# Kernel tuning notes

Measured on AMD Instinct MI355X. Metric: run time of the kernel, lower is better.

## Reference

```python
import jax, jax.numpy as jnp
import numpy as np

N = 384        # number of sentences (paramemory rows)
D = 768        # d_mlp (BERT hidden size)
C = 2          # num_classes


def setup_inputs() -> dict:
    key = jax.random.key(0)
    k1, k2, k3 = jax.random.split(key, 3)
    paramemory = jax.random.normal(k1, (N, D), dtype=jnp.float32)
    # Classifier params (eval mode: dropout p=0.0 -> identity)
    W1 = jax.random.normal(k2, (D, 2 * D), dtype=jnp.float32) * (1.0 / np.sqrt(2 * D))
    b1 = jnp.zeros((D,), dtype=jnp.float32)
    W2 = jax.random.normal(k3, (C, D), dtype=jnp.float32) * (1.0 / np.sqrt(D))
    b2 = jnp.zeros((C,), dtype=jnp.float32)
    return {"paramemory": paramemory, "W1": W1, "b1": b1, "W2": W2, "b2": b2}


def reference(paramemory, W1, b1, W2, b2):
    # Original: cp_mem[i, j] = concat(p[i], p[j]); lin = tanh(cp_mem @ W1.T + b1)
    # Equivalent fused form: split W1 columns into the halves that multiply p[i]
    # and p[j]; the concat+matmul becomes a broadcast-add of two small GEMMs.
    d = paramemory.shape[1]
    A = paramemory @ W1[:, :d].T          # [N, D] contribution of p[i]
    B = paramemory @ W1[:, d:].T          # [N, D] contribution of p[j]
    lin_out = jnp.tanh(A[:, None, :] + B[None, :, :] + b1)  # [N, N, D]
    logits = lin_out @ W2.T + b2          # [N, N, C]
    return logits
```

## Files before the change

kernel.cpp:

```cpp
#include <hip/hip_runtime.h>
#include <stdint.h>

#define NROWS 384
#define DDIM  768
#define NCOL  1536
#define L2E2  2.885390081777927f

#define WS_BT  294912
#define WS_PBF 589824
#define WS_WBF 737280

typedef short bf16x8 __attribute__((ext_vector_type(8)));
typedef float f32x4  __attribute__((ext_vector_type(4)));

__device__ __forceinline__ uint16_t f2bf(float x) {
  const uint32_t u = __float_as_uint(x);
  return (uint16_t)((u + 0x7FFFu + ((u >> 16) & 1u)) >> 16);
}
__device__ __forceinline__ bf16x8 pack8(const float* f) {
  bf16x8 r;
  #pragma unroll
  for (int j = 0; j < 8; ++j) r[j] = (short)f2bf(f[j]);
  return r;
}

__global__ __launch_bounds__(256) void k0_cvt(
    const float* __restrict__ p, const float* __restrict__ W1,
    float* __restrict__ ws) {
  const int t = blockIdx.x * 256 + threadIdx.x;
  const int NP = NROWS * DDIM / 8;
  float f[8];
  if (t < NP) {
    *(float4*)&f[0] = *(const float4*)&p[t * 8];
    *(float4*)&f[4] = *(const float4*)&p[t * 8 + 4];
    *(bf16x8*)((uint16_t*)(ws + WS_PBF) + (size_t)t * 8) = pack8(f);
  } else {
    const int u = t - NP;
    *(float4*)&f[0] = *(const float4*)&W1[(size_t)u * 8];
    *(float4*)&f[4] = *(const float4*)&W1[(size_t)u * 8 + 4];
    *(bf16x8*)((uint16_t*)(ws + WS_WBF) + (size_t)u * 8) = pack8(f);
  }
}

__global__ __launch_bounds__(256) void k1_mfma(
    const float* __restrict__ b1, float* __restrict__ ws) {
  __shared__ float cmb[2][64][4];

  const int lane = threadIdx.x & 63;
  const int w    = threadIdx.x >> 6;
  const int nsub = w & 1;
  const int ksub = w >> 1;
  const int nn   = lane & 15;
  const int quad = lane >> 4;

  const int mbase = blockIdx.y * 16;
  const int nbase = blockIdx.x * 32 + nsub * 16;
  const int g     = nbase >= DDIM;
  const int obase = nbase - g * DDIM;

  const uint16_t* __restrict__ pbf = (const uint16_t*)(ws + WS_PBF);
  const uint16_t* __restrict__ wbf = (const uint16_t*)(ws + WS_WBF);

  const uint16_t* __restrict__ pa =
      pbf + (size_t)(mbase + nn) * DDIM + ksub * 384 + quad * 8;
  const uint16_t* __restrict__ pb =
      wbf + (size_t)(obase + nn) * NCOL + g * DDIM + ksub * 384 + quad * 8;

  f32x4 acc = {0.f, 0.f, 0.f, 0.f};

  #pragma unroll 4
  for (int kk = 0; kk < 384; kk += 32) {
    const bf16x8 a = *(const bf16x8*)&pa[kk];
    const bf16x8 b = *(const bf16x8*)&pb[kk];
    acc = __builtin_amdgcn_mfma_f32_16x16x32_bf16(a, b, acc, 0, 0, 0);
  }

  if (ksub == 1)
    *(float4*)&cmb[nsub][lane][0] = make_float4(acc[0], acc[1], acc[2], acc[3]);
  __syncthreads();
  if (ksub == 0) {
    const float4 o4 = *(const float4*)&cmb[nsub][lane][0];
    float v[4] = {acc[0] + o4.x, acc[1] + o4.y, acc[2] + o4.z, acc[3] + o4.w};
    const int od = obase + nn;
    if (!g) {
      const float bias = b1[od];
      float* __restrict__ A2 = ws;
      #pragma unroll
      for (int r = 0; r < 4; ++r)
        A2[(size_t)(mbase + quad * 4 + r) * DDIM + od] = (v[r] + bias) * L2E2;
    } else {
      float* __restrict__ Bt = ws + WS_BT;
      const int hi = (od >> 2) * NROWS;
      const int lo = od & 3;
      #pragma unroll
      for (int r = 0; r < 4; ++r)
        Bt[(size_t)(hi + mbase + quad * 4 + r) * 4 + lo] = v[r] * L2E2;
    }
  }
}

__global__ __launch_bounds__(256) void k2_fused(
    const float* __restrict__ ws, const float* __restrict__ W2,
    const float* __restrict__ b2, float* __restrict__ out) {
  __shared__ float As[192][16];
  __shared__ float Wsh[192][8];
  __shared__ float part[3][4][64][2];

  const int lane = threadIdx.x & 63;
  const int h    = threadIdx.x >> 6;
  const int i0   = blockIdx.x * 4;
  const int j    = blockIdx.y * 64 + lane;

  for (int u = threadIdx.x; u < 768 + 384; u += 256) {
    if (u < 768) {
      const int row = u / 192, dg = u % 192;
      *(float4*)&As[dg][row * 4] =
          *(const float4*)&ws[(size_t)(i0 + row) * DDIM + dg * 4];
    } else {
      const int v = u - 768, c = v / 192, dg = v % 192;
      *(float4*)&Wsh[dg][c * 4] =
          *(const float4*)&W2[(size_t)c * DDIM + dg * 4];
    }
  }

  const float* __restrict__ w0g = W2 + h * 192;
  const float* __restrict__ w1g = W2 + DDIM + h * 192;
  float sw0 = w0g[lane] + w0g[lane + 64] + w0g[lane + 128];
  float sw1 = w1g[lane] + w1g[lane + 64] + w1g[lane + 128];
  #pragma unroll
  for (int off = 32; off; off >>= 1) {
    sw0 += __shfl_xor(sw0, off);
    sw1 += __shfl_xor(sw1, off);
  }
  __syncthreads();

  const float4* __restrict__ B4 =
      (const float4*)(ws + WS_BT) + (size_t)(h * 48) * NROWS + j;

  f32x4 s0[4] = {{0,0,0,0},{0,0,0,0},{0,0,0,0},{0,0,0,0}};
  f32x4 s1[4] = {{0,0,0,0},{0,0,0,0},{0,0,0,0},{0,0,0,0}};

  #pragma unroll 2
  for (int dg = 0; dg < 48; ++dg) {
    const int dgg = h * 48 + dg;
    const float4 b4  = B4[(size_t)dg * NROWS];
    const float4 w04 = *(const float4*)&Wsh[dgg][0];
    const float4 w14 = *(const float4*)&Wsh[dgg][4];

    #pragma unroll
    for (int row = 0; row < 4; ++row) {
      const float4 av = *(const float4*)&As[dgg][row * 4];
      float e, r;
      e = __builtin_amdgcn_exp2f(av.x + b4.x); r = __builtin_amdgcn_rcpf(e + 1.f);
      s0[row][0] = fmaf(w04.x, r, s0[row][0]); s1[row][0] = fmaf(w14.x, r, s1[row][0]);
      e = __builtin_amdgcn_exp2f(av.y + b4.y); r = __builtin_amdgcn_rcpf(e + 1.f);
      s0[row][1] = fmaf(w04.y, r, s0[row][1]); s1[row][1] = fmaf(w14.y, r, s1[row][1]);
      e = __builtin_amdgcn_exp2f(av.z + b4.z); r = __builtin_amdgcn_rcpf(e + 1.f);
      s0[row][2] = fmaf(w04.z, r, s0[row][2]); s1[row][2] = fmaf(w14.z, r, s1[row][2]);
      e = __builtin_amdgcn_exp2f(av.w + b4.w); r = __builtin_amdgcn_rcpf(e + 1.f);
      s0[row][3] = fmaf(w04.w, r, s0[row][3]); s1[row][3] = fmaf(w14.w, r, s1[row][3]);
    }
  }

  float p0[4], p1[4];
  #pragma unroll
  for (int row = 0; row < 4; ++row) {
    const float S0 = (s0[row][0] + s0[row][1]) + (s0[row][2] + s0[row][3]);
    const float S1 = (s1[row][0] + s1[row][1]) + (s1[row][2] + s1[row][3]);
    p0[row] = fmaf(-2.f, S0, sw0);
    p1[row] = fmaf(-2.f, S1, sw1);
  }

  if (h) {
    #pragma unroll
    for (int row = 0; row < 4; ++row) {
      part[h - 1][row][lane][0] = p0[row];
      part[h - 1][row][lane][1] = p1[row];
    }
  }
  __syncthreads();
  if (!h) {
    #pragma unroll
    for (int row = 0; row < 4; ++row) {
      float2 r2;
      r2.x = p0[row] + part[0][row][lane][0] + part[1][row][lane][0] +
             part[2][row][lane][0] + b2[0];
      r2.y = p1[row] + part[0][row][lane][1] + part[1][row][lane][1] +
             part[2][row][lane][1] + b2[1];
      *(float2*)&out[((size_t)(i0 + row) * NROWS + j) * 2] = r2;
    }
  }
}

extern "C" void kernel_launch(void* const* d_in, const int* in_sizes, int n_in,
                              void* d_out, int out_size, void* d_ws, size_t ws_size,
                              hipStream_t stream) {
  const float* p  = (const float*)d_in[0];
  const float* W1 = (const float*)d_in[1];
  const float* b1 = (const float*)d_in[2];
  const float* W2 = (const float*)d_in[3];
  const float* b2 = (const float*)d_in[4];
  float* out = (float*)d_out;
  float* ws  = (float*)d_ws;

  k0_cvt<<<dim3(720), 256, 0, stream>>>(p, W1, ws);

  dim3 g1(NCOL / 32, NROWS / 16);
  k1_mfma<<<g1, 256, 0, stream>>>(b1, ws);

  dim3 g2(NROWS / 4, NROWS / 64);
  k2_fused<<<g2, 256, 0, stream>>>(ws, W2, b2, out);
}
```

Before: 117.9 us.

## Retile fused tanh-logit kernel to 2x128 tiles with 8-way D split

The fused tanh/logit kernel now uses 512-thread blocks covering 2 i-rows by 128 j-columns, with the D dimension split across 8 waves instead of 4. Each thread evaluates a 2x2 (row, column) tile, so each As/W2 shared-memory read is reused across two column halves rather than four rows. The grid goes from 576 to 576 blocks of doubled size, and the cross-wave reduction grows to 7 partials. The MFMA projection loop also gains two independent accumulators to hide MFMA dependency latency.

```diff
diff --git a/kernel.cpp b/kernel.cpp
--- a/kernel.cpp
+++ b/kernel.cpp
@@ -58,22 +58,24 @@
   const int g     = nbase >= DDIM;
   const int obase = nbase - g * DDIM;
 
-  const uint16_t* __restrict__ pbf = (const uint16_t*)(ws + WS_PBF);
-  const uint16_t* __restrict__ wbf = (const uint16_t*)(ws + WS_WBF);
-
   const uint16_t* __restrict__ pa =
-      pbf + (size_t)(mbase + nn) * DDIM + ksub * 384 + quad * 8;
+      (const uint16_t*)(ws + WS_PBF) + (size_t)(mbase + nn) * DDIM + ksub * 384 + quad * 8;
   const uint16_t* __restrict__ pb =
-      wbf + (size_t)(obase + nn) * NCOL + g * DDIM + ksub * 384 + quad * 8;
-
-  f32x4 acc = {0.f, 0.f, 0.f, 0.f};
-
-  #pragma unroll 4
-  for (int kk = 0; kk < 384; kk += 32) {
-    const bf16x8 a = *(const bf16x8*)&pa[kk];
-    const bf16x8 b = *(const bf16x8*)&pb[kk];
-    acc = __builtin_amdgcn_mfma_f32_16x16x32_bf16(a, b, acc, 0, 0, 0);
-  }
+      (const uint16_t*)(ws + WS_WBF) + (size_t)(obase + nn) * NCOL + g * DDIM + ksub * 384 + quad * 8;
+
+  f32x4 acc0 = {0.f, 0.f, 0.f, 0.f};
+  f32x4 acc1 = {0.f, 0.f, 0.f, 0.f};
+
+  #pragma unroll
+  for (int kk = 0; kk < 384; kk += 64) {
+    const bf16x8 a0 = *(const bf16x8*)&pa[kk];
+    const bf16x8 b0 = *(const bf16x8*)&pb[kk];
+    const bf16x8 a1 = *(const bf16x8*)&pa[kk + 32];
+    const bf16x8 b1v = *(const bf16x8*)&pb[kk + 32];
+    acc0 = __builtin_amdgcn_mfma_f32_16x16x32_bf16(a0, b0, acc0, 0, 0, 0);
+    acc1 = __builtin_amdgcn_mfma_f32_16x16x32_bf16(a1, b1v, acc1, 0, 0, 0);
+  }
+  f32x4 acc = acc0 + acc1;
 
   if (ksub == 1)
     *(float4*)&cmb[nsub][lane][0] = make_float4(acc[0], acc[1], acc[2], acc[3]);
@@ -99,34 +101,36 @@
   }
 }
 
-__global__ __launch_bounds__(256) void k2_fused(
+__global__ __launch_bounds__(512) void k2_fused(
     const float* __restrict__ ws, const float* __restrict__ W2,
     const float* __restrict__ b2, float* __restrict__ out) {
-  __shared__ float As[192][16];
-  __shared__ float Wsh[192][8];
-  __shared__ float part[3][4][64][2];
-
-  const int lane = threadIdx.x & 63;
-  const int h    = threadIdx.x >> 6;
-  const int i0   = blockIdx.x * 4;
-  const int j    = blockIdx.y * 64 + lane;
-
-  for (int u = threadIdx.x; u < 768 + 384; u += 256) {
-    if (u < 768) {
+  __shared__ float As[192][12];
+  __shared__ float Wsh[192][12];
+  __shared__ float part[7][2][2][64][2];
+
+  const int tid  = threadIdx.x;
+  const int lane = tid & 63;
+  const int h    = tid >> 6;
+  const int i0   = blockIdx.x * 2;
+  const int jb   = blockIdx.y * 128;
+  const int j    = jb + lane;
+
+  for (int u = tid; u < 768; u += 512) {
+    if (u < 384) {
       const int row = u / 192, dg = u % 192;
       *(float4*)&As[dg][row * 4] =
           *(const float4*)&ws[(size_t)(i0 + row) * DDIM + dg * 4];
     } else {
-      const int v = u - 768, c = v / 192, dg = v % 192;
+      const int v = u - 384, c = v / 192, dg = v % 192;
       *(float4*)&Wsh[dg][c * 4] =
           *(const float4*)&W2[(size_t)c * DDIM + dg * 4];
     }
   }
 
-  const float* __restrict__ w0g = W2 + h * 192;
-  const float* __restrict__ w1g = W2 + DDIM + h * 192;
-  float sw0 = w0g[lane] + w0g[lane + 64] + w0g[lane + 128];
-  float sw1 = w1g[lane] + w1g[lane + 64] + w1g[lane + 128];
+  const float* __restrict__ w0g = W2 + h * 96;
+  const float* __restrict__ w1g = W2 + DDIM + h * 96;
+  float sw0 = w0g[lane] + (lane < 32 ? w0g[64 + lane] : 0.f);
+  float sw1 = w1g[lane] + (lane < 32 ? w1g[64 + lane] : 0.f);
   #pragma unroll
   for (int off = 32; off; off >>= 1) {
     sw0 += __shfl_xor(sw0, off);
@@ -135,60 +139,79 @@
   __syncthreads();
 
   const float4* __restrict__ B4 =
-      (const float4*)(ws + WS_BT) + (size_t)(h * 48) * NROWS + j;
-
-  f32x4 s0[4] = {{0,0,0,0},{0,0,0,0},{0,0,0,0},{0,0,0,0}};
-  f32x4 s1[4] = {{0,0,0,0},{0,0,0,0},{0,0,0,0},{0,0,0,0}};
+      (const float4*)(ws + WS_BT) + (size_t)(h * 24) * NROWS;
+
+  f32x4 s[2][2][2] = {};
 
   #pragma unroll 2
-  for (int dg = 0; dg < 48; ++dg) {
-    const int dgg = h * 48 + dg;
-    const float4 b4  = B4[(size_t)dg * NROWS];
+  for (int dg = 0; dg < 24; ++dg) {
+    const int dgg = h * 24 + dg;
+    const float4 b4a = B4[(size_t)dg * NROWS + j];
+    const float4 b4b = B4[(size_t)dg * NROWS + j + 64];
+    const float4 av0 = *(const float4*)&As[dgg][0];
+    const float4 av1 = *(const float4*)&As[dgg][4];
     const float4 w04 = *(const float4*)&Wsh[dgg][0];
     const float4 w14 = *(const float4*)&Wsh[dgg][4];
 
     #pragma unroll
-    for (int row = 0; row < 4; ++row) {
-      const float4 av = *(const float4*)&As[dgg][row * 4];
-      float e, r;
-      e = __builtin_amdgcn_exp2f(av.x + b4.x); r = __builtin_amdgcn_rcpf(e + 1.f);
-      s0[row][0] = fmaf(w04.x, r, s0[row][0]); s1[row][0] = fmaf(w14.x, r, s1[row][0]);
-      e = __builtin_amdgcn_exp2f(av.y + b4.y); r = __builtin_amdgcn_rcpf(e + 1.f);
-      s0[row][1] = fmaf(w04.y, r, s0[row][1]); s1[row][1] = fmaf(w14.y, r, s1[row][1]);
-      e = __builtin_amdgcn_exp2f(av.z + b4.z); r = __builtin_amdgcn_rcpf(e + 1.f);
-      s0[row][2] = fmaf(w04.z, r, s0[row][2]); s1[row][2] = fmaf(w14.z, r, s1[row][2]);
-      e = __builtin_amdgcn_exp2f(av.w + b4.w); r = __builtin_amdgcn_rcpf(e + 1.f);
-      s0[row][3] = fmaf(w04.w, r, s0[row][3]); s1[row][3] = fmaf(w14.w, r, s1[row][3]);
-    }
-  }
-
-  float p0[4], p1[4];
-  #pragma unroll
-  for (int row = 0; row < 4; ++row) {
-    const float S0 = (s0[row][0] + s0[row][1]) + (s0[row][2] + s0[row][3]);
-    const float S1 = (s1[row][0] + s1[row][1]) + (s1[row][2] + s1[row][3]);
-    p0[row] = fmaf(-2.f, S0, sw0);
-    p1[row] = fmaf(-2.f, S1, sw1);
-  }
+    for (int rw = 0; rw < 2; ++rw) {
+      const float4 av = rw ? av1 : av0;
+      #pragma unroll
+      for (int jh = 0; jh < 2; ++jh) {
+        const float4 b4 = jh ? b4b : b4a;
+        float e, r;
+        e = __builtin_amdgcn_exp2f(av.x + b4.x); r = __builtin_amdgcn_rcpf(e + 1.f);
+        s[rw][jh][0][0] = fmaf(w04.x, r, s[rw][jh][0][0]);
+        s[rw][jh][1][0] = fmaf(w14.x, r, s[rw][jh][1][0]);
+        e = __builtin_amdgcn_exp2f(av.y + b4.y); r = __builtin_amdgcn_rcpf(e + 1.f);
+        s[rw][jh][0][1] = fmaf(w04.y, r, s[rw][jh][0][1]);
+        s[rw][jh][1][1] = fmaf(w14.y, r, s[rw][jh][1][1]);
+        e = __builtin_amdgcn_exp2f(av.z + b4.z); r = __builtin_amdgcn_rcpf(e + 1.f);
+        s[rw][jh][0][2] = fmaf(w04.z, r, s[rw][jh][0][2]);
+        s[rw][jh][1][2] = fmaf(w14.z, r, s[rw][jh][1][2]);
+        e = __builtin_amdgcn_exp2f(av.w + b4.w); r = __builtin_amdgcn_rcpf(e + 1.f);
+        s[rw][jh][0][3] = fmaf(w04.w, r, s[rw][jh][0][3]);
+        s[rw][jh][1][3] = fmaf(w14.w, r, s[rw][jh][1][3]);
+      }
+    }
+  }
+
+  float pl[2][2][2];
+  #pragma unroll
+  for (int rw = 0; rw < 2; ++rw)
+    #pragma unroll
+    for (int jh = 0; jh < 2; ++jh) {
+      const float S0 = (s[rw][jh][0][0] + s[rw][jh][0][1]) + (s[rw][jh][0][2] + s[rw][jh][0][3]);
+      const float S1 = (s[rw][jh][1][0] + s[rw][jh][1][1]) + (s[rw][jh][1][2] + s[rw][jh][1][3]);
+      pl[rw][jh][0] = fmaf(-2.f, S0, sw0);
+      pl[rw][jh][1] = fmaf(-2.f, S1, sw1);
+    }
 
   if (h) {
     #pragma unroll
-    for (int row = 0; row < 4; ++row) {
-      part[h - 1][row][lane][0] = p0[row];
-      part[h - 1][row][lane][1] = p1[row];
-    }
+    for (int rw = 0; rw < 2; ++rw)
+      #pragma unroll
+      for (int jh = 0; jh < 2; ++jh) {
+        part[h - 1][rw][jh][lane][0] = pl[rw][jh][0];
+        part[h - 1][rw][jh][lane][1] = pl[rw][jh][1];
+      }
   }
   __syncthreads();
-  if (!h) {
-    #pragma unroll
-    for (int row = 0; row < 4; ++row) {
-      float2 r2;
-      r2.x = p0[row] + part[0][row][lane][0] + part[1][row][lane][0] +
-             part[2][row][lane][0] + b2[0];
-      r2.y = p1[row] + part[0][row][lane][1] + part[1][row][lane][1] +
-             part[2][row][lane][1] + b2[1];
-      *(float2*)&out[((size_t)(i0 + row) * NROWS + j) * 2] = r2;
-    }
+  if (h == 0) {
+    #pragma unroll
+    for (int rw = 0; rw < 2; ++rw)
+      #pragma unroll
+      for (int jh = 0; jh < 2; ++jh) {
+        float2 r2;
+        r2.x = pl[rw][jh][0] + b2[0];
+        r2.y = pl[rw][jh][1] + b2[1];
+        #pragma unroll
+        for (int e = 0; e < 7; ++e) {
+          r2.x += part[e][rw][jh][lane][0];
+          r2.y += part[e][rw][jh][lane][1];
+        }
+        *(float2*)&out[((size_t)(i0 + rw) * NROWS + jb + jh * 64 + lane) * 2] = r2;
+      }
   }
 }
 
@@ -208,6 +231,6 @@
   dim3 g1(NCOL / 32, NROWS / 16);
   k1_mfma<<<g1, 256, 0, stream>>>(b1, ws);
 
-  dim3 g2(NROWS / 4, NROWS / 64);
-  k2_fused<<<g2, 256, 0, stream>>>(ws, W2, b2, out);
-}
+  dim3 g2(NROWS / 2, NROWS / 128);
+  k2_fused<<<g2, 512, 0, stream>>>(ws, W2, b2, out);
+}
```

New measurement: 116.2 us. No clear change (-1.5%).
